# Kernel optimization log

Measured on AMD Instinct MI355X. Metric: run time of the kernel, lower is better.

Reference implementation:

```python
import jax, jax.numpy as jnp
import numpy as np

B, N, D, K = 512, 8192, 4096, 8  # B*K must equal D for the original .view to be valid
H = D // 2


def setup_inputs() -> dict:
    key = jax.random.key(0)
    ks = jax.random.split(key, 14)
    s = 1.0 / np.sqrt(D)
    inp = {
        "input_vector": jax.random.normal(ks[0], (B, D), jnp.float32),
        # learned parameters (all nodes active)
        "node_emb": jax.random.normal(ks[1], (N, D), jnp.float32) * 0.1,
        "adj": (jax.random.uniform(ks[2], (N, N), jnp.float32)
                * (jax.random.uniform(ks[3], (N, N), jnp.float32) < 0.01)),
        "Wq": jax.random.normal(ks[4], (D, D), jnp.float32) * s,
        "Wk": jax.random.normal(ks[5], (D, D), jnp.float32) * s,
        "W1": jax.random.normal(ks[6], (D, H), jnp.float32) * s,
        "b1": jnp.zeros((H,), jnp.float32),
        "W2": jax.random.normal(ks[7], (H, D), jnp.float32) * (1.0 / np.sqrt(H)),
        "b2": jnp.zeros((D,), jnp.float32),
        "Wc": jax.random.normal(ks[8], (D, 1), jnp.float32) * s,
        "Wo": jax.random.normal(ks[9], (D, D), jnp.float32) * s,
        "bo": jnp.zeros((D,), jnp.float32),
    }
    return inp


def reference(input_vector, node_emb, adj, Wq, Wk, W1, b1, W2, b2, Wc, Wo, bo):
    x = input_vector  # [B, D]
    # attention retrieval over active nodes (all N active)
    q = x @ Wq                                   # [B, D]
    keys = node_emb @ Wk                         # [N, D]
    scores = (q @ keys.T) / np.sqrt(D)           # [B, N]
    attn = jax.nn.softmax(scores, axis=-1)
    topk_w, topk_i = jax.lax.top_k(attn, K)     # [B, K]

    # vectorized bundle activation (faithful to original, needs B*K == D)
    sel = node_emb[topk_i]                       # [B, K, D]
    msg = adj[topk_i.reshape(-1)] @ node_emb     # [B*K, D]
    t = sel.reshape(-1, D) @ msg.T               # [B*K, B*K]
    bundle_inf = t.T.reshape(B, K, D)
    enh = sel + 0.1 * bundle_inf                 # [B, K, D]

    # activation MLP (exact GELU like torch default) + weighted aggregation
    h = jax.nn.gelu(enh @ W1 + b1, approximate=False) @ W2 + b2
    agg = (h * topk_w[..., None]).sum(axis=1)    # [B, D]

    final = (x + agg) @ Wo + bo                  # [B, D]
    conf = jax.nn.sigmoid(final @ Wc)            # [B, 1]
    return final, conf
```

## Files before the change

### kernel.cpp

```cpp
#include <hip/hip_runtime.h>
#include <hip/hip_bf16.h>
#include <math.h>

using bf16 = __hip_bfloat16;
using u8 = unsigned char;

typedef __attribute__((ext_vector_type(8))) short short8;
typedef __attribute__((ext_vector_type(4))) float f32x4;
typedef __attribute__((ext_vector_type(16))) float f32x16;
typedef __attribute__((ext_vector_type(4))) int int4v;
typedef __attribute__((ext_vector_type(8))) int int32x8;
typedef __attribute__((ext_vector_type(2))) unsigned int uint2v;

static constexpr int Bsz = 512, Nn = 8192, Dd = 4096, Hh = 2048;

enum { EPI_BF16 = 0, EPI_SCALE_F32, EPI_BIAS_BF16, EPI_BIAS_F32,
       EPI_FP8, EPI_ENH_FP8, EPI_GELU_FP8 };

__device__ __forceinline__ u8 f32_to_fp8(float x) {
  const unsigned int u = __float_as_uint(x);
  const unsigned int s = (u >> 24) & 0x80u;
  const float ax = fminf(__uint_as_float(u & 0x7fffffffu), 448.0f);
  const unsigned int au = __float_as_uint(ax);
  unsigned int b;
  if (au >= 0x3c800000u) {
    const unsigned int r = au + 0x7ffffu + ((au >> 20) & 1u);
    b = (((r >> 23) - 120u) << 3) | ((r >> 20) & 7u);
    if (b > 0x7eu) b = 0x7eu;
  } else {
    b = (unsigned int)(int)rintf(ax * 512.0f);
  }
  return (u8)(b | s);
}

__device__ __forceinline__ float fp8_to_f32(u8 b) {
  const int e = (b >> 3) & 15, m = b & 7;
  const float v = e ? __uint_as_float((unsigned)((e + 120) << 23) | ((unsigned)m << 20))
                    : (float)m * 0.001953125f;
  return (b & 0x80) ? -v : v;
}

__device__ __forceinline__ void gload_lds16(const void* g, void* l) {
  __builtin_amdgcn_global_load_lds(
      (const __attribute__((address_space(1))) void*)g,
      (__attribute__((address_space(3))) void*)l, 16, 0, 0);
}

__device__ __forceinline__ void stage_reg(const void* g, char* region,
                                          long grow0, long pitchB, long kbyte,
                                          int wave, int lane) {
  const int rl = lane >> 2, sl = lane & 3;
  const int s = sl ^ ((rl >> 1) & 3);
  const long r0 = (long)(wave << 5) + rl;
  const char* src0 = (const char*)g + (grow0 + r0) * pitchB + kbyte + (s << 4);
  gload_lds16(src0, region + (wave << 11));
  gload_lds16(src0 + 16 * pitchB, region + (wave << 11) + 1024);
}

#define VMCNT2 asm volatile("s_waitcnt vmcnt(2)" ::: "memory")
#define VMCNT4 asm volatile("s_waitcnt vmcnt(4)" ::: "memory")

#define READ_AMX(DST, RG)                                                      \
  _Pragma("unroll") for (int mr = 0; mr < 4; ++mr) {                           \
    const int off0 = ((rowA + mr * 32) << 6) + lSw;                            \
    const int4v lo = *reinterpret_cast<const int4v*>((RG) + off0);             \
    const int4v hi = *reinterpret_cast<const int4v*>((RG) + (off0 ^ 16));      \
    DST[mr] = __builtin_shufflevector(lo, hi, 0, 1, 2, 3, 4, 5, 6, 7);         \
  }

#define READ_BMX(DST, RG)                                                      \
  _Pragma("unroll") for (int nr = 0; nr < 2; ++nr) {                           \
    const int off0 = ((rowB + nr * 32) << 6) + lSw;                            \
    const int4v lo = *reinterpret_cast<const int4v*>((RG) + off0);             \
    const int4v hi = *reinterpret_cast<const int4v*>((RG) + (off0 ^ 16));      \
    DST[nr] = __builtin_shufflevector(lo, hi, 0, 1, 2, 3, 4, 5, 6, 7);         \
  }

#define MFMA_MX(AV, BV)                                                        \
  __builtin_amdgcn_s_setprio(1);                                               \
  _Pragma("unroll") for (int mr = 0; mr < 4; ++mr)                             \
  _Pragma("unroll") for (int nr = 0; nr < 2; ++nr)                             \
    acc[mr][nr] = __builtin_amdgcn_mfma_scale_f32_32x32x64_f8f6f4(             \
        AV[mr], BV[nr], acc[mr][nr], 0, 0, 0, 0x7f7f7f7f, 0, 0x7f7f7f7f);      \
  __builtin_amdgcn_s_setprio(0);

template<int EPI>
__global__ __launch_bounds__(512, 1)
void gemm_mx(const u8* __restrict__ A, const u8* __restrict__ Bt,
             void* __restrict__ Cp, const u8* __restrict__ sel,
             const float* __restrict__ bias, float scale,
             int M, int N, int K)
{
  __shared__ char lds[131072];
  const int tid  = threadIdx.x;
  const int lane = tid & 63;
  const int wave = tid >> 6;
  const int wm = wave >> 2;
  const int wn = wave & 3;

  const int nblk = (M >> 8) * (N >> 8);
  const int q8 = nblk >> 3, r8 = nblk & 7;
  const int xcd = blockIdx.x & 7, pos = blockIdx.x >> 3;
  const int wg = (xcd < r8 ? xcd * (q8 + 1) : r8 * (q8 + 1) + (xcd - r8) * q8) + pos;
  const int ntx = N >> 8;
  const long bcol = (long)(wg % ntx) << 8;
  const long brow = (long)(wg / ntx) << 8;

  const int rowA = wm * 128 + (lane & 31);
  const int rowB = wn * 64 + (lane & 31);
  const int lSw = (((lane >> 5) ^ ((lane >> 2) & 1)) << 5) | (((lane >> 1) & 1) << 4);

  f32x16 acc[4][2] = {};
  const int KT = K >> 7;

  {
    char* const b = (char*)lds;
    stage_reg(Bt, b + 32768, bcol, K, 0,  wave, lane);
    stage_reg(A,  b,         brow, K, 0,  wave, lane);
    stage_reg(Bt, b + 49152, bcol, K, 64, wave, lane);
    stage_reg(A,  b + 16384, brow, K, 64, wave, lane);
  }
  VMCNT2;
  __builtin_amdgcn_s_barrier();

  for (int t = 0; t < KT; ++t) {
    const int c = t & 1;
    char* const buf  = (char*)lds + c * 65536;
    char* const nbuf = (char*)lds + (c ^ 1) * 65536;
    const int tn = (t + 1 < KT) ? (t + 1) : t;
    const long kbn = (long)tn << 7;
    int32x8 aF[4], aG[4], bF[2], bG[2];

    stage_reg(Bt, nbuf + 32768, bcol, K, kbn, wave, lane);
    READ_AMX(aF, buf);
    READ_BMX(bF, buf + 32768);
    READ_BMX(bG, buf + 49152);
    MFMA_MX(aF, bF);
    stage_reg(A, nbuf, brow, K, kbn, wave, lane);
    VMCNT4;
    __builtin_amdgcn_s_barrier();

    stage_reg(Bt, nbuf + 49152, bcol, K, kbn + 64, wave, lane);
    READ_AMX(aG, buf + 16384);
    MFMA_MX(aG, bG);
    stage_reg(A, nbuf + 16384, brow, K, kbn + 64, wave, lane);
    VMCNT2;
    __builtin_amdgcn_s_barrier();
  }

#pragma unroll
  for (int mr = 0; mr < 4; ++mr)
#pragma unroll
  for (int nr = 0; nr < 2; ++nr) {
    const long col = bcol + wn * 64 + nr * 32 + (lane & 31);
#pragma unroll
    for (int reg = 0; reg < 16; ++reg) {
      const long row = brow + wm * 128 + mr * 32 +
                       (reg & 3) + 8 * (reg >> 2) + 4 * (lane >> 5);
      const long idx = row * N + col;
      const float v = acc[mr][nr][reg];
      if constexpr (EPI == EPI_BF16) {
        reinterpret_cast<bf16*>(Cp)[idx] = __float2bfloat16(v);
      } else if constexpr (EPI == EPI_FP8) {
        reinterpret_cast<u8*>(Cp)[idx] = f32_to_fp8(v);
      } else if constexpr (EPI == EPI_ENH_FP8) {
        reinterpret_cast<u8*>(Cp)[idx] = f32_to_fp8(fp8_to_f32(sel[idx]) + 0.1f * v);
      } else if constexpr (EPI == EPI_GELU_FP8) {
        const float tt = v + bias[col];
        reinterpret_cast<u8*>(Cp)[idx] =
            f32_to_fp8(0.5f * tt * (1.0f + erff(tt * 0.7071067811865475f)));
      } else if constexpr (EPI == EPI_BIAS_BF16) {
        reinterpret_cast<bf16*>(Cp)[idx] = __float2bfloat16(v + bias[col]);
      } else {
        reinterpret_cast<float*>(Cp)[idx] = v + bias[col];
      }
    }
  }
}

template<int EPI>
__global__ __launch_bounds__(256)
void gemm_nt(const bf16* __restrict__ A, const bf16* __restrict__ Bt,
             void* __restrict__ Cp, const float* __restrict__ bias, float scale,
             int M, int N, int K)
{
  __shared__ bf16 As[128 * 64];
  __shared__ bf16 Bs[128 * 64];
  const int tid  = threadIdx.x;
  const int lane = tid & 63;
  const int wave = tid >> 6;
  const int wm = wave >> 1, wn = wave & 1;
  const long brow = (long)blockIdx.y * 128;
  const long bcol = (long)blockIdx.x * 128;

  f32x4 acc[4][4] = {};

  for (int k0 = 0; k0 < K; k0 += 64) {
    __syncthreads();
#pragma unroll
    for (int i = 0; i < 4; ++i) {
      const int s  = i * 256 + tid;
      const int r  = s >> 3;
      const int cs = s & 7;
      const int col = ((cs ^ (r & 7)) << 3);
      *reinterpret_cast<short8*>(&As[s << 3]) =
          *reinterpret_cast<const short8*>(&A[(brow + r) * K + k0 + col]);
      *reinterpret_cast<short8*>(&Bs[s << 3]) =
          *reinterpret_cast<const short8*>(&Bt[(bcol + r) * K + k0 + col]);
    }
    __syncthreads();
#pragma unroll
    for (int kk = 0; kk < 2; ++kk) {
      short8 af[4], bq[4];
      const int cc = (kk << 2) + (lane >> 4);
#pragma unroll
      for (int m = 0; m < 4; ++m) {
        const int r = wm * 64 + m * 16 + (lane & 15);
        af[m] = *reinterpret_cast<const short8*>(&As[((r << 3) + (cc ^ (r & 7))) << 3]);
      }
#pragma unroll
      for (int n = 0; n < 4; ++n) {
        const int r = wn * 64 + n * 16 + (lane & 15);
        bq[n] = *reinterpret_cast<const short8*>(&Bs[((r << 3) + (cc ^ (r & 7))) << 3]);
      }
#pragma unroll
      for (int m = 0; m < 4; ++m)
#pragma unroll
        for (int n = 0; n < 4; ++n)
          acc[m][n] = __builtin_amdgcn_mfma_f32_16x16x32_bf16(af[m], bq[n], acc[m][n], 0, 0, 0);
    }
  }

#pragma unroll
  for (int m = 0; m < 4; ++m) {
    const long row0 = brow + wm * 64 + m * 16 + ((lane >> 4) << 2);
#pragma unroll
    for (int n = 0; n < 4; ++n) {
      const long col = bcol + wn * 64 + n * 16 + (lane & 15);
#pragma unroll
      for (int j = 0; j < 4; ++j) {
        const long idx = (row0 + j) * N + col;
        const float v = acc[m][n][j];
        if constexpr (EPI == EPI_BF16) {
          reinterpret_cast<bf16*>(Cp)[idx] = __float2bfloat16(v);
        } else if constexpr (EPI == EPI_SCALE_F32) {
          reinterpret_cast<float*>(Cp)[idx] = v * scale;
        } else if constexpr (EPI == EPI_BIAS_BF16) {
          reinterpret_cast<bf16*>(Cp)[idx] = __float2bfloat16(v + bias[col]);
        } else if constexpr (EPI == EPI_BIAS_F32) {
          reinterpret_cast<float*>(Cp)[idx] = v + bias[col];
        }
      }
    }
  }
}

__global__ __launch_bounds__(256)
void k_convert_bf16(const float* __restrict__ in, bf16* __restrict__ out, long n4)
{
  const long i = (long)blockIdx.x * 256 + threadIdx.x;
  if (i >= n4) return;
  const f32x4 v = *reinterpret_cast<const f32x4*>(&in[i * 4]);
  bf16 o[4] __attribute__((aligned(8)));
#pragma unroll
  for (int j = 0; j < 4; ++j) o[j] = __float2bfloat16(v[j]);
  *reinterpret_cast<uint2v*>(&out[i * 4]) = *reinterpret_cast<uint2v*>(o);
}

__global__ __launch_bounds__(256)
void k_convert_fp8(const float* __restrict__ in, u8* __restrict__ out, long n4)
{
  const long i = (long)blockIdx.x * 256 + threadIdx.x;
  if (i >= n4) return;
  const f32x4 v = *reinterpret_cast<const f32x4*>(&in[i * 4]);
  u8 o[4] __attribute__((aligned(4)));
#pragma unroll
  for (int j = 0; j < 4; ++j) o[j] = f32_to_fp8(v[j]);
  *reinterpret_cast<unsigned int*>(&out[i * 4]) = *reinterpret_cast<unsigned int*>(o);
}

__global__ __launch_bounds__(256)
void k_transpose_bf16(const float* __restrict__ in, bf16* __restrict__ out, int R, int C)
{
  __shared__ float t[64][65];
  const int bc = blockIdx.x << 6;
  const int br = blockIdx.y << 6;
  for (int i = threadIdx.x; i < 4096; i += 256) {
    const int r = i >> 6, c = i & 63;
    t[r][c] = in[(long)(br + r) * C + (bc + c)];
  }
  __syncthreads();
  for (int i = threadIdx.x; i < 4096; i += 256) {
    const int r = i >> 6, c = i & 63;
    out[(long)(bc + r) * R + (br + c)] = __float2bfloat16(t[c][r]);
  }
}

__global__ __launch_bounds__(256)
void k_transpose_fp8(const float* __restrict__ in, u8* __restrict__ out, int R, int C)
{
  __shared__ float t[64][65];
  const int bc = blockIdx.x << 6;
  const int br = blockIdx.y << 6;
  for (int i = threadIdx.x; i < 4096; i += 256) {
    const int r = i >> 6, c = i & 63;
    t[r][c] = in[(long)(br + r) * C + (bc + c)];
  }
  __syncthreads();
  for (int i = threadIdx.x; i < 4096; i += 256) {
    const int r = i >> 6, c = i & 63;
    out[(long)(bc + r) * R + (br + c)] = f32_to_fp8(t[c][r]);
  }
}

__global__ __launch_bounds__(256)
void k_gather_fp8(const float* __restrict__ src, const int* __restrict__ map,
                  u8* __restrict__ dst, int cols)
{
  const long i = (long)blockIdx.x * 256 + threadIdx.x;
  const int cpr = cols >> 2;
  const int row = (int)(i / cpr);
  const int c4  = (int)(i % cpr) << 2;
  const f32x4 v = *reinterpret_cast<const f32x4*>(&src[(long)map[row] * cols + c4]);
  u8 o[4] __attribute__((aligned(4)));
#pragma unroll
  for (int j = 0; j < 4; ++j) o[j] = f32_to_fp8(v[j]);
  *reinterpret_cast<unsigned int*>(&dst[(long)row * cols + c4]) =
      *reinterpret_cast<unsigned int*>(o);
}

__global__ __launch_bounds__(256)
void k_gather_rows8(const u8* __restrict__ src, const int* __restrict__ map,
                    u8* __restrict__ dst, int cols)
{
  const long i = (long)blockIdx.x * 256 + threadIdx.x;
  const int cpr = cols >> 4;
  const int row = (int)(i / cpr);
  const int c16 = (int)(i % cpr) << 4;
  *reinterpret_cast<int4v*>(&dst[(long)row * cols + c16]) =
      *reinterpret_cast<const int4v*>(&src[(long)map[row] * cols + c16]);
}

__global__ __launch_bounds__(256)
void k_softmax_topk(const float* __restrict__ scores, int* __restrict__ tki,
                    float* __restrict__ tkw)
{
  const int b = blockIdx.x;
  const float* row = scores + (long)b * Nn;
  const int tid = threadIdx.x;
  __shared__ float red[8];
  __shared__ float cv[2048];
  __shared__ int   ci[2048];

  float mx = -INFINITY;
  for (int i = tid; i < Nn; i += 256) mx = fmaxf(mx, row[i]);
#pragma unroll
  for (int o = 32; o; o >>= 1) mx = fmaxf(mx, __shfl_down(mx, o));
  if ((tid & 63) == 0) red[tid >> 6] = mx;
  __syncthreads();
  mx = fmaxf(fmaxf(red[0], red[1]), fmaxf(red[2], red[3]));

  float tv[8]; int ti[8];
#pragma unroll
  for (int j = 0; j < 8; ++j) { tv[j] = -INFINITY; ti[j] = 0x7fffffff; }
  float sum = 0.f;
  for (int i = tid; i < Nn; i += 256) {
    const float v = row[i];
    sum += expf(v - mx);
    if (v > tv[7]) {
      tv[7] = v; ti[7] = i;
#pragma unroll
      for (int j = 7; j > 0; --j) {
        const bool sw = (tv[j] > tv[j-1]) || (tv[j] == tv[j-1] && ti[j] < ti[j-1]);
        if (sw) {
          const float fv = tv[j]; tv[j] = tv[j-1]; tv[j-1] = fv;
          const int   iv = ti[j]; ti[j] = ti[j-1]; ti[j-1] = iv;
        }
      }
    }
  }
  float s2 = sum;
#pragma unroll
  for (int o = 32; o; o >>= 1) s2 += __shfl_down(s2, o);
  if ((tid & 63) == 0) red[4 + (tid >> 6)] = s2;

#pragma unroll
  for (int j = 0; j < 8; ++j) { cv[tid * 8 + j] = tv[j]; ci[tid * 8 + j] = ti[j]; }
  __syncthreads();
  const float denom = red[4] + red[5] + red[6] + red[7];

  if (tid < 64) {
    for (int p = 0; p < 8; ++p) {
      float bv = -INFINITY; int bi = 0x7fffffff;
      for (int q = 0; q < 32; ++q) {
        const int slot = tid + (q << 6);
        const float v = cv[slot]; const int id = ci[slot];
        if (v > bv || (v == bv && id < bi)) { bv = v; bi = id; }
      }
#pragma unroll
      for (int o = 32; o; o >>= 1) {
        const float ov = __shfl_xor(bv, o);
        const int   oi = __shfl_xor(bi, o);
        if (ov > bv || (ov == bv && oi < bi)) { bv = ov; bi = oi; }
      }
      if (tid == 0) { tki[b * 8 + p] = bi; tkw[b * 8 + p] = expf(bv - mx) / denom; }
      for (int q = 0; q < 32; ++q) {
        const int slot = tid + (q << 6);
        if (ci[slot] == bi) cv[slot] = -INFINITY;
      }
    }
  }
}

__global__ __launch_bounds__(256)
void k_agg_xa(const float* __restrict__ x, const bf16* __restrict__ hout,
              const float* __restrict__ tkw, bf16* __restrict__ xa)
{
  const long i = (long)blockIdx.x * 256 + threadIdx.x;
  const int b = (int)(i >> 12);
  const int d = (int)(i & 4095);
  float a = x[i];
#pragma unroll
  for (int k = 0; k < 8; ++k)
    a += tkw[b * 8 + k] * __bfloat162float(hout[(((long)b * 8 + k) << 12) + d]);
  xa[i] = __float2bfloat16(a);
}

__global__ __launch_bounds__(256)
void k_conf(const float* __restrict__ fin, const float* __restrict__ Wc,
            float* __restrict__ conf)
{
  const int b = blockIdx.x;
  float s = 0.f;
  for (int d = threadIdx.x; d < Dd; d += 256)
    s += fin[(long)b * Dd + d] * Wc[d];
#pragma unroll
  for (int o = 32; o; o >>= 1) s += __shfl_down(s, o);
  __shared__ float r4[4];
  if ((threadIdx.x & 63) == 0) r4[threadIdx.x >> 6] = s;
  __syncthreads();
  if (threadIdx.x == 0) {
    const float t = r4[0] + r4[1] + r4[2] + r4[3];
    conf[b] = 1.f / (1.f + expf(-t));
  }
}

template<int EPI>
static inline void launch_gemm(const bf16* A, const bf16* Bt, void* C,
                               const float* bias, float scale,
                               int M, int N, int K, hipStream_t st)
{
  gemm_nt<EPI><<<dim3(N / 128, M / 128), 256, 0, st>>>(A, Bt, C, bias, scale, M, N, K);
}

template<int EPI>
static inline void launch_mx(const u8* A, const u8* Bt, void* C,
                             const u8* sel, const float* bias,
                             int M, int N, int K, hipStream_t st)
{
  gemm_mx<EPI><<<dim3((M >> 8) * (N >> 8)), 512, 0, st>>>(A, Bt, C, sel, bias, 1.f, M, N, K);
}

extern "C" void kernel_launch(void* const* d_in, const int* in_sizes, int n_in,
                              void* d_out, int out_size, void* d_ws, size_t ws_size,
                              hipStream_t stream)
{
  const float* x   = (const float*)d_in[0];
  const float* ne  = (const float*)d_in[1];
  const float* adj = (const float*)d_in[2];
  const float* Wq  = (const float*)d_in[3];
  const float* Wk  = (const float*)d_in[4];
  const float* W1  = (const float*)d_in[5];
  const float* b1  = (const float*)d_in[6];
  const float* W2  = (const float*)d_in[7];
  const float* b2  = (const float*)d_in[8];
  const float* Wc  = (const float*)d_in[9];
  const float* Wo  = (const float*)d_in[10];
  const float* bo  = (const float*)d_in[11];
  float* out = (float*)d_out;

  char* ws = (char*)d_ws;
  u8*    ne8   = (u8*)(ws);
  u8*    neT8  = (u8*)(ws + (32ll  << 20));
  u8*    adjG8 = (u8*)(ws + (64ll  << 20));
  bf16*  hout  = (bf16*)(ws + (64ll << 20));
  bf16*  keys  = (bf16*)(ws + (96ll  << 20));
  void*  slotW = (void*)(ws + (160ll << 20));
  u8*    sel8  = (u8*)(ws + (192ll << 20));
  u8*    msg8  = (u8*)(ws + (208ll << 20));
  u8*    hmid8 = msg8;
  float* scores= (float*)(ws + (224ll << 20));
  u8*    enh8  = (u8*)(ws + (224ll << 20));
  bf16*  xbf   = (bf16*)(ws + (240ll << 20));
  bf16*  qbf   = (bf16*)(ws + (244ll << 20));
  bf16*  xa    = (bf16*)(ws + (248ll << 20));
  int*   tki   = (int*)(ws + (252ll << 20));
  float* tkw   = (float*)(ws + (252ll << 20) + 16384);

  const long neN4 = (long)Nn * Dd / 4;
  const long xN4  = (long)Bsz * Dd / 4;

  k_convert_fp8<<<(int)(neN4 / 256), 256, 0, stream>>>(ne, ne8, neN4);
  k_transpose_fp8<<<dim3(64, 64), 256, 0, stream>>>(Wk, (u8*)slotW, Dd, Dd);
  launch_mx<EPI_BF16>(ne8, (u8*)slotW, keys, nullptr, nullptr, Nn, Dd, Dd, stream);
  k_convert_bf16<<<(int)(xN4 / 256), 256, 0, stream>>>(x, xbf, xN4);
  k_transpose_bf16<<<dim3(64, 64), 256, 0, stream>>>(Wq, (bf16*)slotW, Dd, Dd);
  launch_gemm<EPI_BF16>(xbf, (bf16*)slotW, qbf, nullptr, 1.f, Bsz, Dd, Dd, stream);
  launch_gemm<EPI_SCALE_F32>(qbf, keys, scores, nullptr, 1.f / 64.f, Bsz, Nn, Dd, stream);
  k_softmax_topk<<<Bsz, 256, 0, stream>>>(scores, tki, tkw);
  k_gather_rows8<<<(int)((long)4096 * Dd / 16 / 256), 256, 0, stream>>>(ne8, tki, sel8, Dd);
  k_gather_fp8<<<(int)((long)4096 * Nn / 4 / 256), 256, 0, stream>>>(adj, tki, adjG8, Nn);
  k_transpose_fp8<<<dim3(Dd / 64, Nn / 64), 256, 0, stream>>>(ne, neT8, Nn, Dd);
  launch_mx<EPI_FP8>(adjG8, neT8, msg8, nullptr, nullptr, 4096, Dd, Nn, stream);
  launch_mx<EPI_ENH_FP8>(msg8, sel8, enh8, sel8, nullptr, 4096, Dd, Dd, stream);
  k_transpose_fp8<<<dim3(Hh / 64, Dd / 64), 256, 0, stream>>>(W1, (u8*)slotW, Dd, Hh);
  launch_mx<EPI_GELU_FP8>(enh8, (u8*)slotW, hmid8, nullptr, b1, 4096, Hh, Dd, stream);
  k_transpose_fp8<<<dim3(Dd / 64, Hh / 64), 256, 0, stream>>>(W2, (u8*)slotW, Hh, Dd);
  launch_mx<EPI_BIAS_BF16>(hmid8, (u8*)slotW, hout, nullptr, b2, 4096, Dd, Hh, stream);
  k_agg_xa<<<(int)((long)Bsz * Dd / 256), 256, 0, stream>>>(x, hout, tkw, xa);
  k_transpose_bf16<<<dim3(64, 64), 256, 0, stream>>>(Wo, (bf16*)slotW, Dd, Dd);
  launch_gemm<EPI_BIAS_F32>(xa, (bf16*)slotW, out, bo, 1.f, Bsz, Dd, Dd, stream);
  k_conf<<<Bsz, 256, 0, stream>>>(out, Wc, out + (long)Bsz * Dd);
}
```

Before: 1.148 ms.

## Replace double-buffered K pipeline with four-slot ring prefetching three stages ahead

```diff
diff --git a/kernel.cpp b/kernel.cpp
--- a/kernel.cpp
+++ b/kernel.cpp
@@ -57,8 +57,7 @@
   gload_lds16(src0 + 16 * pitchB, region + (wave << 11) + 1024);
 }
 
-#define VMCNT2 asm volatile("s_waitcnt vmcnt(2)" ::: "memory")
-#define VMCNT4 asm volatile("s_waitcnt vmcnt(4)" ::: "memory")
+#define VMCNT8 asm volatile("s_waitcnt vmcnt(8)" ::: "memory")
 
 #define READ_AMX(DST, RG)                                                      \
   _Pragma("unroll") for (int mr = 0; mr < 4; ++mr) {                           \
@@ -110,41 +109,32 @@
   const int rowB = wn * 64 + (lane & 31);
   const int lSw = (((lane >> 5) ^ ((lane >> 2) & 1)) << 5) | (((lane >> 1) & 1) << 4);
 
+  char* const Ar = (char*)lds;
+  char* const Br = (char*)lds + 65536;
+
   f32x16 acc[4][2] = {};
-  const int KT = K >> 7;
-
-  {
-    char* const b = (char*)lds;
-    stage_reg(Bt, b + 32768, bcol, K, 0,  wave, lane);
-    stage_reg(A,  b,         brow, K, 0,  wave, lane);
-    stage_reg(Bt, b + 49152, bcol, K, 64, wave, lane);
-    stage_reg(A,  b + 16384, brow, K, 64, wave, lane);
-  }
-  VMCNT2;
+  const int HT = K >> 6;
+
+#pragma unroll
+  for (int h = 0; h < 3; ++h) {
+    stage_reg(Bt, Br + h * 16384, bcol, K, (long)h << 6, wave, lane);
+    stage_reg(A,  Ar + h * 16384, brow, K, (long)h << 6, wave, lane);
+  }
+  VMCNT8;
   __builtin_amdgcn_s_barrier();
 
-  for (int t = 0; t < KT; ++t) {
-    const int c = t & 1;
-    char* const buf  = (char*)lds + c * 65536;
-    char* const nbuf = (char*)lds + (c ^ 1) * 65536;
-    const int tn = (t + 1 < KT) ? (t + 1) : t;
-    const long kbn = (long)tn << 7;
-    int32x8 aF[4], aG[4], bF[2], bG[2];
-
-    stage_reg(Bt, nbuf + 32768, bcol, K, kbn, wave, lane);
-    READ_AMX(aF, buf);
-    READ_BMX(bF, buf + 32768);
-    READ_BMX(bG, buf + 49152);
+  for (int h = 0; h < HT; ++h) {
+    const int hn = (h + 3 < HT) ? (h + 3) : (HT - 1);
+    const int rg = (h + 3) & 3;
+    stage_reg(Bt, Br + rg * 16384, bcol, K, (long)hn << 6, wave, lane);
+    stage_reg(A,  Ar + rg * 16384, brow, K, (long)hn << 6, wave, lane);
+
+    int32x8 aF[4], bF[2];
+    READ_AMX(aF, Ar + (h & 3) * 16384);
+    READ_BMX(bF, Br + (h & 3) * 16384);
     MFMA_MX(aF, bF);
-    stage_reg(A, nbuf, brow, K, kbn, wave, lane);
-    VMCNT4;
-    __builtin_amdgcn_s_barrier();
-
-    stage_reg(Bt, nbuf + 49152, bcol, K, kbn + 64, wave, lane);
-    READ_AMX(aG, buf + 16384);
-    MFMA_MX(aG, bG);
-    stage_reg(A, nbuf + 16384, brow, K, kbn + 64, wave, lane);
-    VMCNT2;
+
+    VMCNT8;
     __builtin_amdgcn_s_barrier();
   }
 
```

Result: no change. 1.147 ms (-0.1%).
